# Optimization experiments

Hardware: AMD Instinct MI355X
Metric: run time of the kernel (lower is better)

Reference implementation:

```python
import jax, jax.numpy as jnp
import numpy as np

B, D, T = 2048, 1024, 4
L_S1, L_S2, L_T1, L_T2 = 2, 2, 2, 2  # shared1, shared2, task1, task2 stack depths
H = 64  # head width before final scalar output


def setup_inputs() -> dict:
    key = jax.random.key(0)
    ks = jax.random.split(key, 16)
    s = 0.02
    inp = {
        'x': jax.random.normal(ks[0], (B, D), dtype=jnp.float32),
        'batch_task': jax.random.randint(ks[1], (B,), 0, T, dtype=jnp.int32),
        # shared block 1: dim_mlpinput==D so all layers are [D,D]
        'ws1_W': jax.random.normal(ks[2], (L_S1, D, D), dtype=jnp.float32) * s,
        'ws1_b': jax.random.normal(ks[3], (L_S1, D), dtype=jnp.float32) * s,
        # task block 1: per-task stacks [T, L, D, D]
        'wt1_W': jax.random.normal(ks[4], (T, L_T1, D, D), dtype=jnp.float32) * s,
        'wt1_b': jax.random.normal(ks[5], (T, L_T1, D), dtype=jnp.float32) * s,
        # shared block 2
        'ws2_W': jax.random.normal(ks[6], (L_S2, D, D), dtype=jnp.float32) * s,
        'ws2_b': jax.random.normal(ks[7], (L_S2, D), dtype=jnp.float32) * s,
        # task block 2 body
        'wt2_W': jax.random.normal(ks[8], (T, L_T2, D, D), dtype=jnp.float32) * s,
        'wt2_b': jax.random.normal(ks[9], (T, L_T2, D), dtype=jnp.float32) * s,
        # per-task head: D->64 then 64->1
        'h1_W': jax.random.normal(ks[10], (T, D, H), dtype=jnp.float32) * s,
        'h1_b': jax.random.normal(ks[11], (T, H), dtype=jnp.float32) * s,
        'h2_W': jax.random.normal(ks[12], (T, H, 1), dtype=jnp.float32) * s,
        'h2_b': jax.random.normal(ks[13], (T, 1), dtype=jnp.float32) * s,
    }
    return inp


def _lin(h, W, b):
    return h @ W + b


def reference(x, batch_task, ws1_W, ws1_b, wt1_W, wt1_b, ws2_W, ws2_b,
              wt2_W, wt2_b, h1_W, h1_b, h2_W, h2_b):
    # dropout p=0 / eval -> identity. multitask branch of the torch module.
    # shared block 1: first linear, then (relu -> linear) for the rest
    h = _lin(x, ws1_W[0], ws1_b[0])
    for l in range(1, ws1_W.shape[0]):
        h = _lin(jax.nn.relu(h), ws1_W[l], ws1_b[l])

    nT = wt1_W.shape[0]
    mask = jax.nn.one_hot(batch_task, nT, dtype=h.dtype)  # [B, T]

    # task block 1: every task layer is (relu -> linear); combine via task mask
    out = jnp.zeros_like(h)
    for t in range(nT):  # small fixed loop over tasks (expert dispatch)
        r = h
        for l in range(wt1_W.shape[1]):
            r = _lin(jax.nn.relu(r), wt1_W[t, l], wt1_b[t, l])
        out = out + mask[:, t:t + 1] * r
    h = out

    # shared block 2
    h = _lin(h, ws2_W[0], ws2_b[0])
    for l in range(1, ws2_W.shape[0]):
        h = _lin(jax.nn.relu(h), ws2_W[l], ws2_b[l])

    # task block 2: (relu->linear)*L_T2, (relu->linear D->64), then final 64->1 with NO relu
    out2 = jnp.zeros((h.shape[0], 1), dtype=h.dtype)
    for t in range(nT):
        r = h
        for l in range(wt2_W.shape[1]):
            r = _lin(jax.nn.relu(r), wt2_W[t, l], wt2_b[t, l])
        r = _lin(jax.nn.relu(r), h1_W[t], h1_b[t])
        r = _lin(r, h2_W[t], h2_b[t])
        out2 = out2 + mask[:, t:t + 1] * r

    return jax.nn.sigmoid(out2)  # [B, 1]
```

## Files before the change

kernel.cpp:

```cpp
#include <hip/hip_runtime.h>


typedef __attribute__((ext_vector_type(4))) float f32x4;
typedef __attribute__((ext_vector_type(8))) __bf16 bf16x8;
typedef __attribute__((ext_vector_type(4))) unsigned short u16x4;

#define AS1 __attribute__((address_space(1)))
#define AS3 __attribute__((address_space(3)))

static constexpr int B_  = 2048;
static constexpr int D_  = 1024;
static constexpr int T_  = 4;
static constexpr int H_  = 64;
static constexpr int MP_ = 2112;
static constexpr size_t MSZ = (size_t)D_ * D_;

static constexpr size_t OFF_PERM = 0;
static constexpr size_t OFF_SEG  = 8192;
static constexpr size_t OFF_W    = 16384;
static constexpr size_t H1T_ELEM_OFF = 20 * MSZ;
static constexpr size_t W_ELEMS  = 20 * MSZ + (size_t)T_ * H_ * D_;
static constexpr size_t OFF_XP   = OFF_W + W_ELEMS * 2;
static constexpr size_t ACT_BYTES = (size_t)MP_ * D_ * 2;
static constexpr size_t OFF_A0   = OFF_XP + ACT_BYTES;
static constexpr size_t OFF_A1   = OFF_A0 + ACT_BYTES;
static constexpr size_t WS_NEED  = OFF_A1 + ACT_BYTES;

static __device__ __forceinline__ unsigned short f2bf(float f) {
    union { float f; unsigned int u; } v; v.f = f;
    unsigned int r = v.u + 0x7fffu + ((v.u >> 16) & 1u);
    return (unsigned short)(r >> 16);
}

__global__ void perm_kernel(const int* __restrict__ btask,
                            int* __restrict__ perm, int* __restrict__ seg) {
    __shared__ int cnt[T_], cur[T_];
    int tid = threadIdx.x;
    if (tid < T_) cnt[tid] = 0;
    __syncthreads();
    for (int i = tid; i < B_; i += 256) atomicAdd(&cnt[btask[i]], 1);
    __syncthreads();
    if (tid == 0) {
        int s = 0;
        for (int t = 0; t < T_; ++t) {
            seg[t] = s; seg[T_ + t] = cnt[t]; cur[t] = s; s += cnt[t];
        }
    }
    __syncthreads();
    for (int i = tid; i < B_; i += 256) {
        int t = btask[i];
        int p = atomicAdd(&cur[t], 1);
        perm[p] = i;
    }
}

__global__ __launch_bounds__(256)
void transpose_cvt(const float* __restrict__ ws1, const float* __restrict__ wt1,
                   const float* __restrict__ ws2, const float* __restrict__ wt2,
                   const float* __restrict__ h1, unsigned short* __restrict__ wb) {
    int z = blockIdx.z;
    const float* src; unsigned short* dst; int C = D_;
    if (z < 2)       { src = ws1 + (size_t)z * MSZ;        dst = wb + (size_t)z * MSZ; }
    else if (z < 10) { src = wt1 + (size_t)(z - 2) * MSZ;  dst = wb + (size_t)z * MSZ; }
    else if (z < 12) { src = ws2 + (size_t)(z - 10) * MSZ; dst = wb + (size_t)z * MSZ; }
    else if (z < 20) { src = wt2 + (size_t)(z - 12) * MSZ; dst = wb + (size_t)z * MSZ; }
    else { src = h1 + (size_t)(z - 20) * (D_ * H_);
           dst = wb + H1T_ELEM_OFF + (size_t)(z - 20) * (D_ * H_); C = H_; }
    int r0 = blockIdx.y * 64, c0 = blockIdx.x * 64;
    if (c0 >= C) return;
    __shared__ float tile[64][65];
    int tid = threadIdx.x;
#pragma unroll
    for (int i = 0; i < 4; ++i) {
        int idx = i * 256 + tid;
        int fr = idx >> 4, fc = (idx & 15) << 2;
        float4 v = *(const float4*)(src + (size_t)(r0 + fr) * C + c0 + fc);
        tile[fr][fc] = v.x; tile[fr][fc + 1] = v.y; tile[fr][fc + 2] = v.z; tile[fr][fc + 3] = v.w;
    }
    __syncthreads();
#pragma unroll
    for (int i = 0; i < 4; ++i) {
        int idx = i * 256 + tid;
        int orow = idx >> 4, ocb = (idx & 15) << 2;
        u16x4 o = { f2bf(tile[ocb][orow]),     f2bf(tile[ocb + 1][orow]),
                    f2bf(tile[ocb + 2][orow]), f2bf(tile[ocb + 3][orow]) };
        *(u16x4*)(dst + (size_t)(c0 + orow) * D_ + r0 + ocb) = o;
    }
}

__global__ void gather_x(const float* __restrict__ x, const int* __restrict__ perm,
                         unsigned short* __restrict__ xp) {
    int pos = blockIdx.x;
    int src = perm[pos];
    int t = threadIdx.x;
    float4 v = *((const float4*)(x + (size_t)src * D_) + t);
    u16x4 o = { f2bf(v.x), f2bf(v.y), f2bf(v.z), f2bf(v.w) };
    *((u16x4*)(xp + (size_t)pos * D_) + t) = o;
}

template<bool RELU, bool TASK>
__global__ __launch_bounds__(256)
void gemm_pass(const unsigned short* __restrict__ A, const unsigned short* __restrict__ W,
               const float* __restrict__ bias, unsigned short* __restrict__ Out,
               const int* __restrict__ seg, size_t wstride, size_t bstride) {
    __shared__ unsigned short lA[3][64 * 64];
    __shared__ unsigned short lB[3][64 * 64];
    int m0, mend, t = 0;
    if (TASK) {
        t = blockIdx.y >> 5;
        int mt = blockIdx.y & 31;
        int s = seg[t], c = seg[4 + t];
        m0 = s + mt * 64; mend = s + c;
        if (m0 >= mend) return;
    } else { m0 = blockIdx.y * 64; mend = B_; }
    const unsigned short* Wt = W + (size_t)t * wstride;
    const float* bs = bias + (size_t)t * bstride;
    const int n0 = blockIdx.x * 64;

    const int tid = threadIdx.x, wid = tid >> 6, lane = tid & 63;
    const int wm = wid >> 1, wn = wid & 1;
    const int l15 = lane & 15, l4 = lane >> 4;
    const int srow = lane >> 3;
    const int sslot = ((lane & 7) ^ srow) * 16;

    f32x4 acc[2][2] = {};

    auto stage = [&](int kt, int buf) {
        const int k0 = kt * 64;
#pragma unroll
        for (int i = 0; i < 2; ++i) {
            int chunk = wid * 2 + i;
            int row = chunk * 8 + srow;
            const char* sa = (const char*)(A + (size_t)(m0 + row) * D_ + k0) + sslot;
            __builtin_amdgcn_global_load_lds((AS1 void*)sa,
                (AS3 void*)(&lA[buf][0] + (size_t)chunk * 512), 16, 0, 0);
            const char* sb = (const char*)(Wt + (size_t)(n0 + row) * D_ + k0) + sslot;
            __builtin_amdgcn_global_load_lds((AS1 void*)sb,
                (AS3 void*)(&lB[buf][0] + (size_t)chunk * 512), 16, 0, 0);
        }
    };

    auto compute = [&](int buf) {
        const unsigned short* bA = &lA[buf][0];
        const unsigned short* bB = &lB[buf][0];
#pragma unroll
        for (int kk = 0; kk < 2; ++kk) {
            const int swz = (((kk * 4) + l4) ^ (l15 & 7)) * 8;
            bf16x8 af[2], bfr[2];
#pragma unroll
            for (int m = 0; m < 2; ++m)
                af[m] = *(const bf16x8*)(bA + (wm * 32 + m * 16 + l15) * 64 + swz);
#pragma unroll
            for (int n = 0; n < 2; ++n)
                bfr[n] = *(const bf16x8*)(bB + (wn * 32 + n * 16 + l15) * 64 + swz);
#pragma unroll
            for (int m = 0; m < 2; ++m)
#pragma unroll
                for (int n = 0; n < 2; ++n)
                    acc[m][n] = __builtin_amdgcn_mfma_f32_16x16x32_bf16(af[m], bfr[n], acc[m][n], 0, 0, 0);
        }
    };

    stage(0, 0);
    stage(1, 1);
    int bc = 0, bn2 = 2;
#pragma unroll 1
    for (int kt = 0; kt < 14; ++kt) {
        asm volatile("s_waitcnt vmcnt(4)" ::: "memory");
        __builtin_amdgcn_s_barrier();
        stage(kt + 2, bn2);
        compute(bc);
        bc  = (bc  == 2) ? 0 : bc  + 1;
        bn2 = (bn2 == 2) ? 0 : bn2 + 1;
    }
    asm volatile("s_waitcnt vmcnt(4)" ::: "memory");
    __builtin_amdgcn_s_barrier();
    compute(bc);
    bc = (bc == 2) ? 0 : bc + 1;
    asm volatile("s_waitcnt vmcnt(0)" ::: "memory");
    __builtin_amdgcn_s_barrier();
    compute(bc);

#pragma unroll
    for (int n = 0; n < 2; ++n) {
        int col = n0 + wn * 32 + n * 16 + l15;
        float bv = bs[col];
#pragma unroll
        for (int m = 0; m < 2; ++m) {
            int rbase = m0 + wm * 32 + m * 16 + l4 * 4;
#pragma unroll
            for (int j = 0; j < 4; ++j) {
                int row = rbase + j;
                if (!TASK || row < mend) {
                    float v = acc[m][n][j] + bv;
                    if (RELU) v = fmaxf(v, 0.f);
                    Out[(size_t)row * D_ + col] = f2bf(v);
                }
            }
        }
    }
}

__global__ __launch_bounds__(256)
void head_pass(const unsigned short* __restrict__ A, const unsigned short* __restrict__ H1t,
               const float* __restrict__ h1b, const float* __restrict__ h2w,
               const float* __restrict__ h2b, const int* __restrict__ seg,
               const int* __restrict__ perm, float* __restrict__ out) {
    __shared__ unsigned short lA[3][64 * 64];
    __shared__ unsigned short lB[3][64 * 64];
    int t = blockIdx.x >> 5, mt = blockIdx.x & 31;
    int s = seg[t], c = seg[4 + t];
    int m0 = s + mt * 64, mend = s + c;
    if (m0 >= mend) return;
    const unsigned short* Ht = H1t + (size_t)t * (H_ * D_);
    const int tid = threadIdx.x, wid = tid >> 6, lane = tid & 63;
    const int l15 = lane & 15, l4 = lane >> 4;
    const int srow = lane >> 3;
    const int sslot = ((lane & 7) ^ srow) * 16;
    f32x4 acc[4] = {};

    auto stage = [&](int kt, int buf) {
        const int k0 = kt * 64;
#pragma unroll
        for (int i = 0; i < 2; ++i) {
            int chunk = wid * 2 + i;
            int row = chunk * 8 + srow;
            const char* sa = (const char*)(A + (size_t)(m0 + row) * D_ + k0) + sslot;
            __builtin_amdgcn_global_load_lds((AS1 void*)sa,
                (AS3 void*)(&lA[buf][0] + (size_t)chunk * 512), 16, 0, 0);
            const char* sb = (const char*)(Ht + (size_t)row * D_ + k0) + sslot;
            __builtin_amdgcn_global_load_lds((AS1 void*)sb,
                (AS3 void*)(&lB[buf][0] + (size_t)chunk * 512), 16, 0, 0);
        }
    };
    auto compute = [&](int buf) {
#pragma unroll
        for (int kk = 0; kk < 2; ++kk) {
            const int swz = (((kk * 4) + l4) ^ (l15 & 7)) * 8;
            bf16x8 af = *(const bf16x8*)(&lA[buf][0] + (wid * 16 + l15) * 64 + swz);
#pragma unroll
            for (int n = 0; n < 4; ++n) {
                bf16x8 bfr = *(const bf16x8*)(&lB[buf][0] + (n * 16 + l15) * 64 + swz);
                acc[n] = __builtin_amdgcn_mfma_f32_16x16x32_bf16(af, bfr, acc[n], 0, 0, 0);
            }
        }
    };

    stage(0, 0);
    stage(1, 1);
    int bc = 0, bn2 = 2;
#pragma unroll 1
    for (int kt = 0; kt < 14; ++kt) {
        asm volatile("s_waitcnt vmcnt(4)" ::: "memory");
        __builtin_amdgcn_s_barrier();
        stage(kt + 2, bn2);
        compute(bc);
        bc  = (bc  == 2) ? 0 : bc  + 1;
        bn2 = (bn2 == 2) ? 0 : bn2 + 1;
    }
    asm volatile("s_waitcnt vmcnt(4)" ::: "memory");
    __builtin_amdgcn_s_barrier();
    compute(bc);
    bc = (bc == 2) ? 0 : bc + 1;
    asm volatile("s_waitcnt vmcnt(0)" ::: "memory");
    __builtin_amdgcn_s_barrier();
    compute(bc);

    float part[4] = {0.f, 0.f, 0.f, 0.f};
#pragma unroll
    for (int n = 0; n < 4; ++n) {
        int col = n * 16 + l15;
        float b1 = h1b[t * H_ + col];
        float w2 = h2w[t * H_ + col];
#pragma unroll
        for (int j = 0; j < 4; ++j) part[j] += (acc[n][j] + b1) * w2;
    }
#pragma unroll
    for (int msk = 1; msk < 16; msk <<= 1)
#pragma unroll
        for (int j = 0; j < 4; ++j) part[j] += __shfl_xor(part[j], msk);
    if (l15 == 0) {
        float b2 = h2b[t];
#pragma unroll
        for (int j = 0; j < 4; ++j) {
            int row = m0 + wid * 16 + l4 * 4 + j;
            if (row < mend) {
                int orig = perm[row];
                out[orig] = 1.f / (1.f + expf(-(part[j] + b2)));
            }
        }
    }
}

extern "C" void kernel_launch(void* const* d_in, const int* in_sizes, int n_in,
                              void* d_out, int out_size, void* d_ws, size_t ws_size,
                              hipStream_t stream) {
    (void)in_sizes; (void)n_in; (void)out_size;
    if (ws_size < WS_NEED) return;

    const float* x    = (const float*)d_in[0];
    const int*   bt   = (const int*)d_in[1];
    const float* ws1W = (const float*)d_in[2];
    const float* ws1b = (const float*)d_in[3];
    const float* wt1W = (const float*)d_in[4];
    const float* wt1b = (const float*)d_in[5];
    const float* ws2W = (const float*)d_in[6];
    const float* ws2b = (const float*)d_in[7];
    const float* wt2W = (const float*)d_in[8];
    const float* wt2b = (const float*)d_in[9];
    const float* h1W  = (const float*)d_in[10];
    const float* h1b  = (const float*)d_in[11];
    const float* h2W  = (const float*)d_in[12];
    const float* h2b  = (const float*)d_in[13];

    char* ws = (char*)d_ws;
    int* perm = (int*)(ws + OFF_PERM);
    int* seg  = (int*)(ws + OFF_SEG);
    unsigned short* wb = (unsigned short*)(ws + OFF_W);
    unsigned short* xp = (unsigned short*)(ws + OFF_XP);
    unsigned short* a0 = (unsigned short*)(ws + OFF_A0);
    unsigned short* a1 = (unsigned short*)(ws + OFF_A1);

    perm_kernel<<<1, 256, 0, stream>>>(bt, perm, seg);
    transpose_cvt<<<dim3(16, 16, 24), 256, 0, stream>>>(ws1W, wt1W, ws2W, wt2W, h1W, wb);
    gather_x<<<B_, 256, 0, stream>>>(x, perm, xp);

    dim3 gs(16, 32), gt(16, 128);
    gemm_pass<true,  false><<<gs, 256, 0, stream>>>(xp, wb + 0 * MSZ,  ws1b + 0,  a0, seg, 0, 0);
    gemm_pass<true,  false><<<gs, 256, 0, stream>>>(a0, wb + 1 * MSZ,  ws1b + D_, a1, seg, 0, 0);
    gemm_pass<true,  true ><<<gt, 256, 0, stream>>>(a1, wb + 2 * MSZ,  wt1b + 0,  a0, seg, 2 * MSZ, 2 * D_);
    gemm_pass<false, true ><<<gt, 256, 0, stream>>>(a0, wb + 3 * MSZ,  wt1b + D_, a1, seg, 2 * MSZ, 2 * D_);
    gemm_pass<true,  false><<<gs, 256, 0, stream>>>(a1, wb + 10 * MSZ, ws2b + 0,  a0, seg, 0, 0);
    gemm_pass<true,  false><<<gs, 256, 0, stream>>>(a0, wb + 11 * MSZ, ws2b + D_, a1, seg, 0, 0);
    gemm_pass<true,  true ><<<gt, 256, 0, stream>>>(a1, wb + 12 * MSZ, wt2b + 0,  a0, seg, 2 * MSZ, 2 * D_);
    gemm_pass<true,  true ><<<gt, 256, 0, stream>>>(a0, wb + 13 * MSZ, wt2b + D_, a1, seg, 2 * MSZ, 2 * D_);
    head_pass<<<dim3(128), 256, 0, stream>>>(a1, wb + H1T_ELEM_OFF, h1b, h2W, h2b, seg, perm, (float*)d_out);
}
```

Baseline: 271.2 us.

## Compute each 64x64 GEMM tile with a single wavefront and drop barriers

Shrinks each GEMM workgroup from four wavefronts to one. That single wave stages all 64 rows of A and W itself and accumulates the full 64x64 output tile in a 4x4 grid of MFMA accumulators. Because only one wave touches LDS, the per-iteration s_barrier calls go away and the vmcnt waits are raised to cover 16 outstanding loads per stage. This removes barrier cost and the duplicated fragment loads, but each CU now has far fewer waves to hide memory latency, and MFMA work is spread across fewer SIMDs.

```diff
diff --git a/kernel.cpp b/kernel.cpp
--- a/kernel.cpp
+++ b/kernel.cpp
@@ -99,7 +99,7 @@
 }
 
 template<bool RELU, bool TASK>
-__global__ __launch_bounds__(256)
+__global__ __launch_bounds__(64)
 void gemm_pass(const unsigned short* __restrict__ A, const unsigned short* __restrict__ W,
                const float* __restrict__ bias, unsigned short* __restrict__ Out,
                const int* __restrict__ seg, size_t wstride, size_t bstride) {
@@ -117,26 +117,29 @@
     const float* bs = bias + (size_t)t * bstride;
     const int n0 = blockIdx.x * 64;
 
-    const int tid = threadIdx.x, wid = tid >> 6, lane = tid & 63;
-    const int wm = wid >> 1, wn = wid & 1;
+    const int lane = threadIdx.x & 63;
     const int l15 = lane & 15, l4 = lane >> 4;
     const int srow = lane >> 3;
     const int sslot = ((lane & 7) ^ srow) * 16;
 
-    f32x4 acc[2][2] = {};
+    f32x4 acc[4][4] = {};
+
+    const char* Abase = (const char*)(A + (size_t)m0 * D_) + (size_t)srow * (D_ * 2) + sslot;
+    const char* Bbase = (const char*)(Wt + (size_t)n0 * D_) + (size_t)srow * (D_ * 2) + sslot;
 
     auto stage = [&](int kt, int buf) {
-        const int k0 = kt * 64;
-#pragma unroll
-        for (int i = 0; i < 2; ++i) {
-            int chunk = wid * 2 + i;
-            int row = chunk * 8 + srow;
-            const char* sa = (const char*)(A + (size_t)(m0 + row) * D_ + k0) + sslot;
+        const size_t k0b = (size_t)kt * 128;
+#pragma unroll
+        for (int c = 0; c < 8; ++c) {
+            const char* sa = Abase + (size_t)c * (8 * D_ * 2) + k0b;
             __builtin_amdgcn_global_load_lds((AS1 void*)sa,
-                (AS3 void*)(&lA[buf][0] + (size_t)chunk * 512), 16, 0, 0);
-            const char* sb = (const char*)(Wt + (size_t)(n0 + row) * D_ + k0) + sslot;
+                (AS3 void*)(&lA[buf][0] + (size_t)c * 512), 16, 0, 0);
+        }
+#pragma unroll
+        for (int c = 0; c < 8; ++c) {
+            const char* sb = Bbase + (size_t)c * (8 * D_ * 2) + k0b;
             __builtin_amdgcn_global_load_lds((AS1 void*)sb,
-                (AS3 void*)(&lB[buf][0] + (size_t)chunk * 512), 16, 0, 0);
+                (AS3 void*)(&lB[buf][0] + (size_t)c * 512), 16, 0, 0);
         }
     };
 
@@ -146,17 +149,17 @@
 #pragma unroll
         for (int kk = 0; kk < 2; ++kk) {
             const int swz = (((kk * 4) + l4) ^ (l15 & 7)) * 8;
-            bf16x8 af[2], bfr[2];
-#pragma unroll
-            for (int m = 0; m < 2; ++m)
-                af[m] = *(const bf16x8*)(bA + (wm * 32 + m * 16 + l15) * 64 + swz);
-#pragma unroll
-            for (int n = 0; n < 2; ++n)
-                bfr[n] = *(const bf16x8*)(bB + (wn * 32 + n * 16 + l15) * 64 + swz);
-#pragma unroll
-            for (int m = 0; m < 2; ++m)
-#pragma unroll
-                for (int n = 0; n < 2; ++n)
+            bf16x8 af[4], bfr[4];
+#pragma unroll
+            for (int m = 0; m < 4; ++m)
+                af[m] = *(const bf16x8*)(bA + (m * 16 + l15) * 64 + swz);
+#pragma unroll
+            for (int n = 0; n < 4; ++n)
+                bfr[n] = *(const bf16x8*)(bB + (n * 16 + l15) * 64 + swz);
+#pragma unroll
+            for (int m = 0; m < 4; ++m)
+#pragma unroll
+                for (int n = 0; n < 4; ++n)
                     acc[m][n] = __builtin_amdgcn_mfma_f32_16x16x32_bf16(af[m], bfr[n], acc[m][n], 0, 0, 0);
         }
     };
@@ -166,28 +169,25 @@
     int bc = 0, bn2 = 2;
 #pragma unroll 1
     for (int kt = 0; kt < 14; ++kt) {
-        asm volatile("s_waitcnt vmcnt(4)" ::: "memory");
-        __builtin_amdgcn_s_barrier();
+        asm volatile("s_waitcnt vmcnt(16)" ::: "memory");
         stage(kt + 2, bn2);
         compute(bc);
         bc  = (bc  == 2) ? 0 : bc  + 1;
         bn2 = (bn2 == 2) ? 0 : bn2 + 1;
     }
-    asm volatile("s_waitcnt vmcnt(4)" ::: "memory");
-    __builtin_amdgcn_s_barrier();
+    asm volatile("s_waitcnt vmcnt(16)" ::: "memory");
     compute(bc);
     bc = (bc == 2) ? 0 : bc + 1;
     asm volatile("s_waitcnt vmcnt(0)" ::: "memory");
-    __builtin_amdgcn_s_barrier();
     compute(bc);
 
 #pragma unroll
-    for (int n = 0; n < 2; ++n) {
-        int col = n0 + wn * 32 + n * 16 + l15;
+    for (int n = 0; n < 4; ++n) {
+        int col = n0 + n * 16 + l15;
         float bv = bs[col];
 #pragma unroll
-        for (int m = 0; m < 2; ++m) {
-            int rbase = m0 + wm * 32 + m * 16 + l4 * 4;
+        for (int m = 0; m < 4; ++m) {
+            int rbase = m0 + m * 16 + l4 * 4;
 #pragma unroll
             for (int j = 0; j < 4; ++j) {
                 int row = rbase + j;
@@ -326,13 +326,13 @@
     gather_x<<<B_, 256, 0, stream>>>(x, perm, xp);
 
     dim3 gs(16, 32), gt(16, 128);
-    gemm_pass<true,  false><<<gs, 256, 0, stream>>>(xp, wb + 0 * MSZ,  ws1b + 0,  a0, seg, 0, 0);
-    gemm_pass<true,  false><<<gs, 256, 0, stream>>>(a0, wb + 1 * MSZ,  ws1b + D_, a1, seg, 0, 0);
-    gemm_pass<true,  true ><<<gt, 256, 0, stream>>>(a1, wb + 2 * MSZ,  wt1b + 0,  a0, seg, 2 * MSZ, 2 * D_);
-    gemm_pass<false, true ><<<gt, 256, 0, stream>>>(a0, wb + 3 * MSZ,  wt1b + D_, a1, seg, 2 * MSZ, 2 * D_);
-    gemm_pass<true,  false><<<gs, 256, 0, stream>>>(a1, wb + 10 * MSZ, ws2b + 0,  a0, seg, 0, 0);
-    gemm_pass<true,  false><<<gs, 256, 0, stream>>>(a0, wb + 11 * MSZ, ws2b + D_, a1, seg, 0, 0);
-    gemm_pass<true,  true ><<<gt, 256, 0, stream>>>(a1, wb + 12 * MSZ, wt2b + 0,  a0, seg, 2 * MSZ, 2 * D_);
-    gemm_pass<true,  true ><<<gt, 256, 0, stream>>>(a0, wb + 13 * MSZ, wt2b + D_, a1, seg, 2 * MSZ, 2 * D_);
+    gemm_pass<true,  false><<<gs, 64, 0, stream>>>(xp, wb + 0 * MSZ,  ws1b + 0,  a0, seg, 0, 0);
+    gemm_pass<true,  false><<<gs, 64, 0, stream>>>(a0, wb + 1 * MSZ,  ws1b + D_, a1, seg, 0, 0);
+    gemm_pass<true,  true ><<<gt, 64, 0, stream>>>(a1, wb + 2 * MSZ,  wt1b + 0,  a0, seg, 2 * MSZ, 2 * D_);
+    gemm_pass<false, true ><<<gt, 64, 0, stream>>>(a0, wb + 3 * MSZ,  wt1b + D_, a1, seg, 2 * MSZ, 2 * D_);
+    gemm_pass<true,  false><<<gs, 64, 0, stream>>>(a1, wb + 10 * MSZ, ws2b + 0,  a0, seg, 0, 0);
+    gemm_pass<true,  false><<<gs, 64, 0, stream>>>(a0, wb + 11 * MSZ, ws2b + D_, a1, seg, 0, 0);
+    gemm_pass<true,  true ><<<gt, 64, 0, stream>>>(a1, wb + 12 * MSZ, wt2b + 0,  a0, seg, 2 * MSZ, 2 * D_);
+    gemm_pass<true,  true ><<<gt, 64, 0, stream>>>(a0, wb + 13 * MSZ, wt2b + D_, a1, seg, 2 * MSZ, 2 * D_);
     head_pass<<<dim3(128), 256, 0, stream>>>(a1, wb + H1T_ELEM_OFF, h1b, h2W, h2b, seg, perm, (float*)d_out);
 }
```

New measurement: 355.0 us. 30.9% more time.

## Remap GEMM blocks to XCD-aware order and deepen LDS pipeline to four stages

Applied to the files above, without the earlier changes.

The 2D GEMM grids become a 1D grid whose block index is decoded so that the eight consecutive block IDs, which round-robin across the eight XCDs, map to distinct M panels while each XCD sweeps every N tile of its panels. This is meant to keep A rows in each XCD's L2. For task GEMMs the mapping is shifted by each segment's base panel. The LDS ring grows from three to four buffers with three tiles in flight, and launch bounds now ask for two blocks per CU. gather_x is remapped the same way. The larger LDS footprint (64KB per block) may limit occupancy, and the remap is fragile if segment offsets are not 64-aligned.

```diff
diff --git a/kernel.cpp b/kernel.cpp
--- a/kernel.cpp
+++ b/kernel.cpp
@@ -90,7 +90,9 @@
 
 __global__ void gather_x(const float* __restrict__ x, const int* __restrict__ perm,
                          unsigned short* __restrict__ xp) {
-    int pos = blockIdx.x;
+    int bid = blockIdx.x;
+    int panel = (bid & 7) + (((bid >> 3) & 3) << 3);
+    int pos = (panel << 6) + (bid >> 5);
     int src = perm[pos];
     int t = threadIdx.x;
     float4 v = *((const float4*)(x + (size_t)src * D_) + t);
@@ -99,23 +101,36 @@
 }
 
 template<bool RELU, bool TASK>
-__global__ __launch_bounds__(256)
+__global__ __launch_bounds__(256, 2)
 void gemm_pass(const unsigned short* __restrict__ A, const unsigned short* __restrict__ W,
                const float* __restrict__ bias, unsigned short* __restrict__ Out,
                const int* __restrict__ seg, size_t wstride, size_t bstride) {
-    __shared__ unsigned short lA[3][64 * 64];
-    __shared__ unsigned short lB[3][64 * 64];
-    int m0, mend, t = 0;
+    __shared__ unsigned short lA[4][4096];
+    __shared__ unsigned short lB[4][4096];
+    const int bid = blockIdx.x;
+    const int x = bid & 7;
+    int m0, mend, n0, t = 0;
     if (TASK) {
-        t = blockIdx.y >> 5;
-        int mt = blockIdx.y & 31;
+        int q = bid >> 3;
+        t = q >> 6;
+        int qq = q & 63;
+        n0 = (qq & 15) << 6;
+        int j = qq >> 4;
         int s = seg[t], c = seg[4 + t];
-        m0 = s + mt * 64; mend = s + c;
+        int bp = s >> 6;
+        int mt = ((x - bp) & 7) + (j << 3);
+        m0 = s + (mt << 6);
+        mend = s + c;
         if (m0 >= mend) return;
-    } else { m0 = blockIdx.y * 64; mend = B_; }
+    } else {
+        int q = bid >> 3;
+        int mp = x + ((q >> 4) << 3);
+        n0 = (q & 15) << 6;
+        m0 = mp << 6;
+        mend = B_;
+    }
     const unsigned short* Wt = W + (size_t)t * wstride;
     const float* bs = bias + (size_t)t * bstride;
-    const int n0 = blockIdx.x * 64;
 
     const int tid = threadIdx.x, wid = tid >> 6, lane = tid & 63;
     const int wm = wid >> 1, wn = wid & 1;
@@ -163,20 +178,22 @@
 
     stage(0, 0);
     stage(1, 1);
-    int bc = 0, bn2 = 2;
+    stage(2, 2);
+    int bc = 0, bn3 = 3;
 #pragma unroll 1
-    for (int kt = 0; kt < 14; ++kt) {
-        asm volatile("s_waitcnt vmcnt(4)" ::: "memory");
+    for (int kt = 0; kt < 13; ++kt) {
+        asm volatile("s_waitcnt vmcnt(8)" ::: "memory");
         __builtin_amdgcn_s_barrier();
-        stage(kt + 2, bn2);
+        stage(kt + 3, bn3);
         compute(bc);
-        bc  = (bc  == 2) ? 0 : bc  + 1;
-        bn2 = (bn2 == 2) ? 0 : bn2 + 1;
-    }
+        bc = (bc + 1) & 3; bn3 = (bn3 + 1) & 3;
+    }
+    asm volatile("s_waitcnt vmcnt(8)" ::: "memory");
+    __builtin_amdgcn_s_barrier();
+    compute(bc); bc = (bc + 1) & 3;
     asm volatile("s_waitcnt vmcnt(4)" ::: "memory");
     __builtin_amdgcn_s_barrier();
-    compute(bc);
-    bc = (bc == 2) ? 0 : bc + 1;
+    compute(bc); bc = (bc + 1) & 3;
     asm volatile("s_waitcnt vmcnt(0)" ::: "memory");
     __builtin_amdgcn_s_barrier();
     compute(bc);
@@ -206,8 +223,8 @@
                const float* __restrict__ h1b, const float* __restrict__ h2w,
                const float* __restrict__ h2b, const int* __restrict__ seg,
                const int* __restrict__ perm, float* __restrict__ out) {
-    __shared__ unsigned short lA[3][64 * 64];
-    __shared__ unsigned short lB[3][64 * 64];
+    __shared__ unsigned short lA[3][4096];
+    __shared__ unsigned short lB[3][4096];
     int t = blockIdx.x >> 5, mt = blockIdx.x & 31;
     int s = seg[t], c = seg[4 + t];
     int m0 = s + mt * 64, mend = s + c;
@@ -325,14 +342,13 @@
     transpose_cvt<<<dim3(16, 16, 24), 256, 0, stream>>>(ws1W, wt1W, ws2W, wt2W, h1W, wb);
     gather_x<<<B_, 256, 0, stream>>>(x, perm, xp);
 
-    dim3 gs(16, 32), gt(16, 128);
-    gemm_pass<true,  false><<<gs, 256, 0, stream>>>(xp, wb + 0 * MSZ,  ws1b + 0,  a0, seg, 0, 0);
-    gemm_pass<true,  false><<<gs, 256, 0, stream>>>(a0, wb + 1 * MSZ,  ws1b + D_, a1, seg, 0, 0);
-    gemm_pass<true,  true ><<<gt, 256, 0, stream>>>(a1, wb + 2 * MSZ,  wt1b + 0,  a0, seg, 2 * MSZ, 2 * D_);
-    gemm_pass<false, true ><<<gt, 256, 0, stream>>>(a0, wb + 3 * MSZ,  wt1b + D_, a1, seg, 2 * MSZ, 2 * D_);
-    gemm_pass<true,  false><<<gs, 256, 0, stream>>>(a1, wb + 10 * MSZ, ws2b + 0,  a0, seg, 0, 0);
-    gemm_pass<true,  false><<<gs, 256, 0, stream>>>(a0, wb + 11 * MSZ, ws2b + D_, a1, seg, 0, 0);
-    gemm_pass<true,  true ><<<gt, 256, 0, stream>>>(a1, wb + 12 * MSZ, wt2b + 0,  a0, seg, 2 * MSZ, 2 * D_);
-    gemm_pass<true,  true ><<<gt, 256, 0, stream>>>(a0, wb + 13 * MSZ, wt2b + D_, a1, seg, 2 * MSZ, 2 * D_);
+    gemm_pass<true,  false><<<512, 256, 0, stream>>>(xp, wb + 0 * MSZ,  ws1b + 0,  a0, seg, 0, 0);
+    gemm_pass<true,  false><<<512, 256, 0, stream>>>(a0, wb + 1 * MSZ,  ws1b + D_, a1, seg, 0, 0);
+    gemm_pass<true,  true ><<<2048, 256, 0, stream>>>(a1, wb + 2 * MSZ,  wt1b + 0,  a0, seg, 2 * MSZ, 2 * D_);
+    gemm_pass<false, true ><<<2048, 256, 0, stream>>>(a0, wb + 3 * MSZ,  wt1b + D_, a1, seg, 2 * MSZ, 2 * D_);
+    gemm_pass<true,  false><<<512, 256, 0, stream>>>(a1, wb + 10 * MSZ, ws2b + 0,  a0, seg, 0, 0);
+    gemm_pass<true,  false><<<512, 256, 0, stream>>>(a0, wb + 11 * MSZ, ws2b + D_, a1, seg, 0, 0);
+    gemm_pass<true,  true ><<<2048, 256, 0, stream>>>(a1, wb + 12 * MSZ, wt2b + 0,  a0, seg, 2 * MSZ, 2 * D_);
+    gemm_pass<true,  true ><<<2048, 256, 0, stream>>>(a0, wb + 13 * MSZ, wt2b + D_, a1, seg, 2 * MSZ, 2 * D_);
     head_pass<<<dim3(128), 256, 0, stream>>>(a1, wb + H1T_ELEM_OFF, h1b, h2W, h2b, seg, perm, (float*)d_out);
 }
```

Result: slower. 302.1 us (+11.4%).
